# Optimization experiments

Hardware: AMD Instinct MI355X
Metric: run time of the kernel (lower is better)

## Reference

```python
import jax, jax.numpy as jnp
import numpy as np

jax.config.update("jax_enable_x64", True)

N_NODES = 1_000_000
N_EDGES = 16_000_000
N_FEAT = 8
N_LABELS = 16

# odd 64-bit mixing constants (fit in signed int64)
_C1 = jnp.int64(6364136223846793005)
_C2 = jnp.int64(1442695040888963407)
_C3 = jnp.int64(2862933555777941757)
_C4 = jnp.int64(3202034522624059733)
_P_TUPLE = jnp.int64(1000003)  # CPython tuple-hash style prime


def setup_inputs() -> dict:
    key = jax.random.key(0)
    k1, k2 = jax.random.split(key)
    x = jax.random.randint(k1, (N_NODES, N_FEAT), 0, N_LABELS, dtype=jnp.int64)
    edge_index = jax.random.randint(k2, (2, N_EDGES), 0, N_NODES, dtype=jnp.int64)
    return {"x": x, "edge_index": edge_index}


def _mix(h, c1, c2):
    # splitmix-style avalanche; int64 arithmetic wraps, which is fine for hashing
    h = h * c1
    h = h ^ (h >> 31)
    h = h * c2
    return h ^ (h >> 29)


def reference(x, edge_index):
    """One Weisfeiler-Lehman refinement step.

    Faithful to WLConvMultiFeature: each node's new label is determined by
    (own feature tuple, sorted multiset of neighbor feature tuples), relabeled
    to contiguous ids in order of first appearance over nodes 0..N-1.
    Python tuple-hashing is replaced by a vectorized 64-bit hash; the sorted
    neighbor tuple is replaced by an order-invariant (commutative) multiset
    hash, which induces the same node partition up to hash collisions.
    """
    N = x.shape[0]

    # --- hash each feature row -> single int64 label (stand-in for tuple(row))
    lab = jnp.zeros((N,), jnp.int64)
    for j in range(x.shape[1]):  # small fixed loop over feature columns
        lab = lab * _P_TUPLE + x[:, j]
    lab = _mix(lab, _C1, _C2)

    # --- commutative multiset hash of neighbor labels per destination node
    src, dst = edge_index[0], edge_index[1]
    nl = lab[src]  # neighbor (source) labels per edge, shape (E,)
    s1 = jax.ops.segment_sum(_mix(nl, _C1, _C2), dst, num_segments=N)
    s2 = jax.ops.segment_sum(_mix(nl, _C3, _C4), dst, num_segments=N)

    # --- combine own label with neighbor multiset hash
    h = _mix(lab * _C3 + s1, _C1, _C2) ^ _mix(s2 + lab, _C3, _C4)

    # --- relabel hashes to contiguous ids in first-appearance order
    order = jnp.argsort(h, stable=True)          # stable -> first occurrence first
    hs = h[order]
    is_new = jnp.concatenate([jnp.ones((1,), bool), hs[1:] != hs[:-1]])
    gid_sorted = jnp.cumsum(is_new.astype(jnp.int64)) - 1  # group id per sorted pos
    gid = jnp.zeros((N,), jnp.int64).at[order].set(gid_sorted)
    # first original index at which each group appears (padded groups -> int64 max)
    first_idx = jax.ops.segment_min(order, gid_sorted, num_segments=N)
    rank_order = jnp.argsort(first_idx)          # groups sorted by first appearance
    rank = jnp.zeros((N,), jnp.int64).at[rank_order].set(jnp.arange(N, dtype=jnp.int64))
    return rank[gid]
```

## Files before the change

kernel.cpp:

```cpp
#include <hip/hip_runtime.h>
#include <stdint.h>


#define KC1 6364136223846793005ULL
#define KC2 1442695040888963407ULL
#define KC3 2862933555777941757ULL
#define KC4 3202034522624059733ULL
#define KPT 1000003ULL

#define TBL_BITS 21
#define TBL (1u << TBL_BITS)
#define TMASK (TBL - 1u)
#define KEMPTY 0xFFFFFFFFFFFFFFFFULL
#define SIGMASK 0xFFFFFFFFFFF00000ULL

#define BK_SHIFT 12
#define BK_NODES 4096
#define NBK_MAX 256
#define NPARTX 8
#define NPARTS 4
#define NPARTS_LOG 2
#define PCAP 2132u
#define OVFCAP 32768u

#define TILE 16384
#define SUBP 4

typedef int iv4 __attribute__((ext_vector_type(4)));

__device__ __forceinline__ uint64_t mix64(uint64_t h, uint64_t a, uint64_t b) {
    h *= a;
    h ^= (uint64_t)(((int64_t)h) >> 31);
    h *= b;
    h ^= (uint64_t)(((int64_t)h) >> 29);
    return h;
}

__device__ __forceinline__ uint32_t tslot(uint64_t k) {
    return (uint32_t)((k * 0x9E3779B97F4A7C15ULL) >> (64 - TBL_BITS));
}

__device__ __forceinline__ uint32_t psel(uint32_t src, uint32_t M) {
    uint32_t p = (uint32_t)(((uint64_t)src * (uint64_t)M) >> 38);
    return p < (NPARTS - 1) ? p : (NPARTS - 1);
}

__global__ void k_lab(const int* __restrict__ x, uint64_t* __restrict__ lab, int N, int F) {
    int i = blockIdx.x * blockDim.x + threadIdx.x;
    if (i >= N) return;
    const int* row = x + (size_t)i * (size_t)F;
    uint64_t l = 0;
    for (int j = 0; j < F; ++j) l = l * KPT + (uint64_t)(int64_t)row[j];
    lab[i] = mix64(l, KC1, KC2);
}

__global__ __launch_bounds__(1024)
void k_scatter(const int* __restrict__ ei, uint32_t* __restrict__ binned,
               uint32_t* __restrict__ cursor, unsigned long long* __restrict__ ovf,
               unsigned int* __restrict__ ovf_cnt, int E, int NBK, int chunk,
               uint32_t M) {
    __shared__ uint32_t stageRec[TILE];
    __shared__ unsigned short stageCell[TILE];
    __shared__ uint32_t hist[NPARTS * NBK_MAX];
    __shared__ uint32_t cstart[NPARTS * NBK_MAX];
    __shared__ uint32_t lbrun[NPARTS * NBK_MAX];
    const int ncl = NPARTS * NBK;
    const int part = blockIdx.x & (NPARTX - 1);
    const int tid = threadIdx.x;
    const int b0 = blockIdx.x * chunk;
    const int b1 = min(E, b0 + chunk);
    if (b0 >= b1) return;

    if (tid < ncl) hist[tid] = 0;
    __syncthreads();

    for (int tb = b0; tb < b1; tb += TILE) {
        const int tE = min(TILE, b1 - tb);
        uint32_t rc[SUBP * 4];
        uint32_t meta[SUBP * 4];
#pragma unroll
        for (int sidx = 0; sidx < SUBP; ++sidx) {
            const int base = tb + sidx * 4096 + tid * 4;
            int ss[4], dd[4];
            int m = 0;
            if (base + 4 <= min(b1, tb + TILE)) {
                iv4 s4 = __builtin_nontemporal_load((const iv4*)(ei + base));
                iv4 d4 = __builtin_nontemporal_load((const iv4*)(ei + (size_t)E + base));
                ss[0]=s4.x; ss[1]=s4.y; ss[2]=s4.z; ss[3]=s4.w;
                dd[0]=d4.x; dd[1]=d4.y; dd[2]=d4.z; dd[3]=d4.w;
                m = 4;
            } else {
                int lim = min(b1, tb + TILE) - base;
                m = lim > 0 ? (lim < 4 ? lim : 4) : 0;
                for (int j = 0; j < m; ++j) {
                    ss[j] = ei[base + j];
                    dd[j] = ei[(size_t)E + base + j];
                }
            }
#pragma unroll
            for (int j = 0; j < 4; ++j) {
                const int k = sidx * 4 + j;
                if (j < m) {
                    uint32_t bk = (uint32_t)dd[j] >> BK_SHIFT;
                    uint32_t cell = (bk << NPARTS_LOG) | psel((uint32_t)ss[j], M);
                    uint32_t pos = atomicAdd(&hist[cell], 1u);
                    rc[k] = ((uint32_t)(dd[j] & (BK_NODES - 1)) << 20) | (uint32_t)ss[j];
                    meta[k] = (cell << 14) | pos;
                } else {
                    meta[k] = 0xFFFFFFFFu;
                }
            }
        }
        __syncthreads();
        cstart[tid] = (tid < ncl) ? hist[tid] : 0u;
        __syncthreads();
        for (int off = 1; off < 1024; off <<= 1) {
            uint32_t t = (tid >= off) ? cstart[tid - off] : 0u;
            __syncthreads();
            cstart[tid] += t;
            __syncthreads();
        }
        if (tid < ncl) {
            uint32_t c = hist[tid];
            cstart[tid] -= c;
            lbrun[tid] = c ? atomicAdd(&cursor[part * ncl + tid], c) : 0u;
        }
        __syncthreads();
#pragma unroll
        for (int k = 0; k < SUBP * 4; ++k) {
            if (meta[k] != 0xFFFFFFFFu) {
                uint32_t cell = meta[k] >> 14;
                uint32_t p = cstart[cell] + (meta[k] & 0x3FFFu);
                stageRec[p] = rc[k];
                stageCell[p] = (unsigned short)cell;
            }
        }
        __syncthreads();
        for (int i = tid; i < tE; i += 1024) {
            uint32_t rec = stageRec[i];
            uint32_t c = stageCell[i];
            uint32_t idx = lbrun[c] + ((uint32_t)i - cstart[c]);
            if (idx < PCAP) {
                binned[((size_t)part * ncl + c) * PCAP + idx] = rec;
            } else {
                unsigned int o = atomicAdd(ovf_cnt, 1u);
                if (o < OVFCAP) ovf[o] = ((unsigned long long)(c >> NPARTS_LOG) << 32) | rec;
            }
        }
        if (tid < ncl) hist[tid] = 0;
        __syncthreads();
    }
}

__device__ __forceinline__ void acc_rec(unsigned long long* s1,
                                        const uint64_t* __restrict__ lab,
                                        uint32_t rec) {
    uint64_t nl = lab[rec & 0xFFFFFu];
    atomicAdd(&s1[rec >> 20], (unsigned long long)mix64(nl, KC1, KC2));
}

__global__ __launch_bounds__(1024)
void k_accum(const uint32_t* __restrict__ binned, const uint32_t* __restrict__ cursor,
             const unsigned long long* __restrict__ ovf, const unsigned int* __restrict__ ovf_cnt,
             const uint64_t* __restrict__ lab, unsigned long long* __restrict__ table,
             uint32_t* __restrict__ slot32, int N, int NBK) {
    __shared__ unsigned long long s1[BK_NODES];
    const int ncl = NPARTS * NBK;
    int b = blockIdx.x;
    for (int t = threadIdx.x; t < BK_NODES; t += blockDim.x) s1[t] = 0ULL;
    __syncthreads();
    const int xp = threadIdx.x >> 7;
    const int lt = threadIdx.x & 127;
    for (int sp = 0; sp < NPARTS; ++sp) {
        const uint32_t cell = ((uint32_t)b << NPARTS_LOG) | (uint32_t)sp;
        const size_t cidx = (size_t)xp * ncl + cell;
        uint32_t cnt = cursor[cidx];
        if (cnt > PCAP) cnt = PCAP;
        const uint32_t* seg = binned + cidx * PCAP;
        uint32_t i = (uint32_t)lt * 4u;
        for (; i + 3u * 512u + 4u <= cnt; i += 4u * 512u) {
            iv4 r0 = __builtin_nontemporal_load((const iv4*)(seg + i));
            iv4 r1 = __builtin_nontemporal_load((const iv4*)(seg + i + 512u));
            iv4 r2 = __builtin_nontemporal_load((const iv4*)(seg + i + 1024u));
            iv4 r3 = __builtin_nontemporal_load((const iv4*)(seg + i + 1536u));
            uint32_t rr[16];
            rr[0]=(uint32_t)r0.x;  rr[1]=(uint32_t)r0.y;  rr[2]=(uint32_t)r0.z;  rr[3]=(uint32_t)r0.w;
            rr[4]=(uint32_t)r1.x;  rr[5]=(uint32_t)r1.y;  rr[6]=(uint32_t)r1.z;  rr[7]=(uint32_t)r1.w;
            rr[8]=(uint32_t)r2.x;  rr[9]=(uint32_t)r2.y;  rr[10]=(uint32_t)r2.z; rr[11]=(uint32_t)r2.w;
            rr[12]=(uint32_t)r3.x; rr[13]=(uint32_t)r3.y; rr[14]=(uint32_t)r3.z; rr[15]=(uint32_t)r3.w;
            uint64_t lv[16];
#pragma unroll
            for (int k = 0; k < 16; ++k) lv[k] = lab[rr[k] & 0xFFFFFu];
#pragma unroll
            for (int k = 0; k < 16; ++k)
                atomicAdd(&s1[rr[k] >> 20], (unsigned long long)mix64(lv[k], KC1, KC2));
        }
        for (; i < cnt; i += 512u) {
            if (i + 4u <= cnt) {
                iv4 r4 = __builtin_nontemporal_load((const iv4*)(seg + i));
                acc_rec(s1, lab, (uint32_t)r4.x);
                acc_rec(s1, lab, (uint32_t)r4.y);
                acc_rec(s1, lab, (uint32_t)r4.z);
                acc_rec(s1, lab, (uint32_t)r4.w);
            } else {
                for (uint32_t j = i; j < cnt; ++j) acc_rec(s1, lab, seg[j]);
            }
        }
        __syncthreads();
    }
    uint32_t oc = *ovf_cnt;
    if (oc > OVFCAP) oc = OVFCAP;
    for (uint32_t i = threadIdx.x; i < oc; i += blockDim.x) {
        unsigned long long r = ovf[i];
        if ((uint32_t)(r >> 32) == (uint32_t)b) acc_rec(s1, lab, (uint32_t)r);
    }
    __syncthreads();
    int node0 = b << BK_SHIFT;
    for (int t = threadIdx.x; t < BK_NODES; t += blockDim.x) {
        int node = node0 + t;
        if (node < N) {
            uint64_t l = lab[node];
            uint64_t s = (uint64_t)s1[t];
            uint64_t h = mix64(l * KC3 + s, KC1, KC2) ^ mix64(s + l, KC3, KC4);
            uint64_t entry = (h & SIGMASK) | (uint64_t)(uint32_t)node;
            uint32_t slot = tslot(h);
            for (;;) {
                unsigned long long cur = table[slot];
                if (cur == KEMPTY) {
                    unsigned long long prev =
                        atomicCAS(&table[slot], KEMPTY, (unsigned long long)entry);
                    if (prev == KEMPTY) break;
                    cur = prev;
                }
                if ((cur & SIGMASK) == (entry & SIGMASK)) {
                    atomicMin(&table[slot], (unsigned long long)entry);
                    break;
                }
                slot = (slot + 1u) & TMASK;
            }
            slot32[node] = slot;
        }
    }
}

__global__ __launch_bounds__(1024)
void k_lookup_scan(const uint32_t* __restrict__ slot32, const unsigned long long* __restrict__ table,
                   unsigned int* __restrict__ rep, int* __restrict__ incl,
                   int* __restrict__ bsums, int N) {
    __shared__ int wsum[16];
    int tid = threadIdx.x;
    int lane = tid & 63;
    int wid = tid >> 6;
    int i = blockIdx.x * 1024 + tid;
    int v = 0;
    if (i < N) {
        unsigned long long e = table[slot32[i]];
        unsigned int r = (unsigned int)(e & 0xFFFFFu);
        rep[i] = r;
        v = (r == (unsigned int)i) ? 1 : 0;
    }
    int s = v;
#pragma unroll
    for (int off = 1; off < 64; off <<= 1) {
        int t = __shfl_up(s, off, 64);
        if (lane >= off) s += t;
    }
    if (lane == 63) wsum[wid] = s;
    __syncthreads();
    if (wid == 0) {
        int w = (lane < 16) ? wsum[lane] : 0;
#pragma unroll
        for (int off = 1; off < 16; off <<= 1) {
            int t = __shfl_up(w, off, 64);
            if (lane >= off) w += t;
        }
        if (lane < 16) wsum[lane] = w;
    }
    __syncthreads();
    int inclv = s + ((wid > 0) ? wsum[wid - 1] : 0);
    if (i < N) incl[i] = inclv;
    if (tid == 1023) bsums[blockIdx.x] = inclv;
}

__global__ void k_scan2(const int* __restrict__ bsums, int* __restrict__ boffs, int NB) {
    __shared__ int sm[1024];
    int tid = threadIdx.x;
    int v = (tid < NB) ? bsums[tid] : 0;
    sm[tid] = v;
    __syncthreads();
    for (int off = 1; off < 1024; off <<= 1) {
        int t = (tid >= off) ? sm[tid - off] : 0;
        __syncthreads();
        sm[tid] += t;
        __syncthreads();
    }
    if (tid < NB) boffs[tid] = sm[tid] - v;
}

__global__ void k_final(const unsigned int* __restrict__ rep, const int* __restrict__ incl,
                        const int* __restrict__ boffs, int* __restrict__ out, int N) {
    int i = blockIdx.x * blockDim.x + threadIdx.x;
    if (i >= N) return;
    unsigned int r = rep[i];
    out[i] = incl[r] + boffs[r >> 10] - 1;
}

extern "C" void kernel_launch(void* const* d_in, const int* in_sizes, int n_in,
                              void* d_out, int out_size, void* d_ws, size_t ws_size,
                              hipStream_t stream) {
    const int* x  = (const int*)d_in[0];
    const int* ei = (const int*)d_in[1];
    int N = out_size;
    int F = in_sizes[0] / N;
    int E = in_sizes[1] / 2;
    int* out = (int*)d_out;

    int NBK = (N + BK_NODES - 1) >> BK_SHIFT;
    uint32_t PSZ = (uint32_t)((N + NPARTS - 1) / NPARTS);
    uint32_t M = (uint32_t)(((1ULL << 38) + PSZ - 1) / PSZ);

    char* w = (char*)d_ws;
    uint64_t* lab = (uint64_t*)w;                        w += (size_t)N * 8;
    uint32_t* slot32 = (uint32_t*)w;                     w += (size_t)N * 4;
    uint32_t* cursor = (uint32_t*)w;                     w += (size_t)NPARTX * NPARTS * NBK_MAX * 4;
    unsigned int* ovf_cnt = (unsigned int*)w;            w += 16;
    unsigned long long* ovf = (unsigned long long*)w;    w += (size_t)OVFCAP * 8;
    unsigned long long* table = (unsigned long long*)w;  w += (size_t)TBL * 8;
    uint32_t* binned = (uint32_t*)w;
    char* a = (char*)binned;
    unsigned int* rep = (unsigned int*)a;                a += (size_t)N * 4;
    int* incl = (int*)a;                                 a += (size_t)N * 4;
    int* bsums = (int*)a;                                a += 1024 * 4;
    int* boffs = (int*)a;                                a += 1024 * 4;

    int nb = (N + 255) / 256;
    int NB = (N + 1023) / 1024;
    int SCB = 256;
    int chunk = ((E + SCB - 1) / SCB + 3) & ~3;

    (void)hipMemsetAsync(cursor, 0, (size_t)NPARTX * NPARTS * NBK_MAX * 4 + 16, stream);
    (void)hipMemsetAsync(table, 0xFF, (size_t)TBL * 8, stream);
    k_lab<<<nb, 256, 0, stream>>>(x, lab, N, F);
    k_scatter<<<SCB, 1024, 0, stream>>>(ei, binned, cursor, ovf, ovf_cnt, E, NBK, chunk, M);
    k_accum<<<NBK, 1024, 0, stream>>>(binned, cursor, ovf, ovf_cnt, lab, table, slot32, N, NBK);
    k_lookup_scan<<<NB, 1024, 0, stream>>>(slot32, table, rep, incl, bsums, N);
    k_scan2<<<1, 1024, 0, stream>>>(bsums, boffs, NB);
    k_final<<<nb, 256, 0, stream>>>(rep, incl, boffs, out, N);
}
```

Measured before the change: 431.4 us.

## Shrink scatter tile, use wave-shuffle scan, precompute bin addresses, simplify accum loop

The scatter kernel halves its tile and staging depth. It replaces the 10-step shared-memory block scan with a wave-level shuffle scan plus a small cross-wave scan. Final global bin addresses and overflow handling are now computed before staging, so the write-out loop only copies packed 64-bit address/record pairs. The accumulate kernel drops its 16-wide manual unroll for a simpler unroll-2 loop and removes the per-partition barrier, which cuts register pressure and synchronisation but may reduce memory-level parallelism.

```diff
diff --git a/kernel.cpp b/kernel.cpp
--- a/kernel.cpp
+++ b/kernel.cpp
@@ -23,8 +23,8 @@
 #define PCAP 2132u
 #define OVFCAP 32768u
 
-#define TILE 16384
-#define SUBP 4
+#define TILE 8192
+#define SUBP 2
 
 typedef int iv4 __attribute__((ext_vector_type(4)));
 
@@ -59,14 +59,17 @@
                uint32_t* __restrict__ cursor, unsigned long long* __restrict__ ovf,
                unsigned int* __restrict__ ovf_cnt, int E, int NBK, int chunk,
                uint32_t M) {
-    __shared__ uint32_t stageRec[TILE];
-    __shared__ unsigned short stageCell[TILE];
+    __shared__ unsigned long long stagePk[TILE];
     __shared__ uint32_t hist[NPARTS * NBK_MAX];
     __shared__ uint32_t cstart[NPARTS * NBK_MAX];
     __shared__ uint32_t lbrun[NPARTS * NBK_MAX];
+    __shared__ uint32_t wsum[16];
     const int ncl = NPARTS * NBK;
     const int part = blockIdx.x & (NPARTX - 1);
     const int tid = threadIdx.x;
+    const int lane = tid & 63;
+    const int wid = tid >> 6;
+    const size_t partBase = (size_t)part * ncl * PCAP;
     const int b0 = blockIdx.x * chunk;
     const int b1 = min(E, b0 + chunk);
     if (b0 >= b1) return;
@@ -76,6 +79,7 @@
 
     for (int tb = b0; tb < b1; tb += TILE) {
         const int tE = min(TILE, b1 - tb);
+        const int lim = min(b1, tb + TILE);
         uint32_t rc[SUBP * 4];
         uint32_t meta[SUBP * 4];
 #pragma unroll
@@ -83,15 +87,15 @@
             const int base = tb + sidx * 4096 + tid * 4;
             int ss[4], dd[4];
             int m = 0;
-            if (base + 4 <= min(b1, tb + TILE)) {
+            if (base + 4 <= lim) {
                 iv4 s4 = __builtin_nontemporal_load((const iv4*)(ei + base));
                 iv4 d4 = __builtin_nontemporal_load((const iv4*)(ei + (size_t)E + base));
                 ss[0]=s4.x; ss[1]=s4.y; ss[2]=s4.z; ss[3]=s4.w;
                 dd[0]=d4.x; dd[1]=d4.y; dd[2]=d4.z; dd[3]=d4.w;
                 m = 4;
             } else {
-                int lim = min(b1, tb + TILE) - base;
-                m = lim > 0 ? (lim < 4 ? lim : 4) : 0;
+                int r = lim - base;
+                m = r > 0 ? (r < 4 ? r : 4) : 0;
                 for (int j = 0; j < m; ++j) {
                     ss[j] = ei[base + j];
                     dd[j] = ei[(size_t)E + base + j];
@@ -105,47 +109,61 @@
                     uint32_t cell = (bk << NPARTS_LOG) | psel((uint32_t)ss[j], M);
                     uint32_t pos = atomicAdd(&hist[cell], 1u);
                     rc[k] = ((uint32_t)(dd[j] & (BK_NODES - 1)) << 20) | (uint32_t)ss[j];
-                    meta[k] = (cell << 14) | pos;
+                    meta[k] = (cell << 13) | pos;
                 } else {
                     meta[k] = 0xFFFFFFFFu;
                 }
             }
         }
         __syncthreads();
-        cstart[tid] = (tid < ncl) ? hist[tid] : 0u;
-        __syncthreads();
-        for (int off = 1; off < 1024; off <<= 1) {
-            uint32_t t = (tid >= off) ? cstart[tid - off] : 0u;
-            __syncthreads();
-            cstart[tid] += t;
-            __syncthreads();
-        }
+        uint32_t v = (tid < ncl) ? hist[tid] : 0u;
+        uint32_t s = v;
+#pragma unroll
+        for (int off = 1; off < 64; off <<= 1) {
+            uint32_t t = __shfl_up(s, off, 64);
+            if (lane >= off) s += t;
+        }
+        if (lane == 63) wsum[wid] = s;
+        __syncthreads();
+        if (wid == 0) {
+            uint32_t w = (lane < 16) ? wsum[lane] : 0u;
+#pragma unroll
+            for (int off = 1; off < 16; off <<= 1) {
+                uint32_t t = __shfl_up(w, off, 64);
+                if (lane >= off) w += t;
+            }
+            if (lane < 16) wsum[lane] = w;
+        }
+        __syncthreads();
+        uint32_t incl = s + ((wid > 0) ? wsum[wid - 1] : 0u);
         if (tid < ncl) {
-            uint32_t c = hist[tid];
-            cstart[tid] -= c;
-            lbrun[tid] = c ? atomicAdd(&cursor[part * ncl + tid], c) : 0u;
+            cstart[tid] = incl - v;
+            lbrun[tid] = v ? atomicAdd(&cursor[part * ncl + tid], v) : 0u;
         }
         __syncthreads();
 #pragma unroll
         for (int k = 0; k < SUBP * 4; ++k) {
             if (meta[k] != 0xFFFFFFFFu) {
-                uint32_t cell = meta[k] >> 14;
-                uint32_t p = cstart[cell] + (meta[k] & 0x3FFFu);
-                stageRec[p] = rc[k];
-                stageCell[p] = (unsigned short)cell;
+                uint32_t cell = meta[k] >> 13;
+                uint32_t pos  = meta[k] & 0x1FFFu;
+                uint32_t idx = lbrun[cell] + pos;
+                uint32_t p = cstart[cell] + pos;
+                if (idx < PCAP) {
+                    stagePk[p] = ((unsigned long long)(cell * PCAP + idx) << 32) | rc[k];
+                } else {
+                    unsigned int o = atomicAdd(ovf_cnt, 1u);
+                    if (o < OVFCAP)
+                        ovf[o] = ((unsigned long long)(cell >> NPARTS_LOG) << 32) | rc[k];
+                    stagePk[p] = 0xFFFFFFFF00000000ULL | rc[k];
+                }
             }
         }
         __syncthreads();
         for (int i = tid; i < tE; i += 1024) {
-            uint32_t rec = stageRec[i];
-            uint32_t c = stageCell[i];
-            uint32_t idx = lbrun[c] + ((uint32_t)i - cstart[c]);
-            if (idx < PCAP) {
-                binned[((size_t)part * ncl + c) * PCAP + idx] = rec;
-            } else {
-                unsigned int o = atomicAdd(ovf_cnt, 1u);
-                if (o < OVFCAP) ovf[o] = ((unsigned long long)(c >> NPARTS_LOG) << 32) | rec;
-            }
+            unsigned long long pk = stagePk[i];
+            uint32_t addr = (uint32_t)(pk >> 32);
+            if (addr != 0xFFFFFFFFu)
+                binned[partBase + addr] = (uint32_t)pk;
         }
         if (tid < ncl) hist[tid] = 0;
         __syncthreads();
@@ -177,25 +195,8 @@
         uint32_t cnt = cursor[cidx];
         if (cnt > PCAP) cnt = PCAP;
         const uint32_t* seg = binned + cidx * PCAP;
-        uint32_t i = (uint32_t)lt * 4u;
-        for (; i + 3u * 512u + 4u <= cnt; i += 4u * 512u) {
-            iv4 r0 = __builtin_nontemporal_load((const iv4*)(seg + i));
-            iv4 r1 = __builtin_nontemporal_load((const iv4*)(seg + i + 512u));
-            iv4 r2 = __builtin_nontemporal_load((const iv4*)(seg + i + 1024u));
-            iv4 r3 = __builtin_nontemporal_load((const iv4*)(seg + i + 1536u));
-            uint32_t rr[16];
-            rr[0]=(uint32_t)r0.x;  rr[1]=(uint32_t)r0.y;  rr[2]=(uint32_t)r0.z;  rr[3]=(uint32_t)r0.w;
-            rr[4]=(uint32_t)r1.x;  rr[5]=(uint32_t)r1.y;  rr[6]=(uint32_t)r1.z;  rr[7]=(uint32_t)r1.w;
-            rr[8]=(uint32_t)r2.x;  rr[9]=(uint32_t)r2.y;  rr[10]=(uint32_t)r2.z; rr[11]=(uint32_t)r2.w;
-            rr[12]=(uint32_t)r3.x; rr[13]=(uint32_t)r3.y; rr[14]=(uint32_t)r3.z; rr[15]=(uint32_t)r3.w;
-            uint64_t lv[16];
-#pragma unroll
-            for (int k = 0; k < 16; ++k) lv[k] = lab[rr[k] & 0xFFFFFu];
-#pragma unroll
-            for (int k = 0; k < 16; ++k)
-                atomicAdd(&s1[rr[k] >> 20], (unsigned long long)mix64(lv[k], KC1, KC2));
-        }
-        for (; i < cnt; i += 512u) {
+#pragma unroll 2
+        for (uint32_t i = (uint32_t)lt * 4u; i < cnt; i += 512u) {
             if (i + 4u <= cnt) {
                 iv4 r4 = __builtin_nontemporal_load((const iv4*)(seg + i));
                 acc_rec(s1, lab, (uint32_t)r4.x);
@@ -206,7 +207,6 @@
                 for (uint32_t j = i; j < cnt; ++j) acc_rec(s1, lab, seg[j]);
             }
         }
-        __syncthreads();
     }
     uint32_t oc = *ovf_cnt;
     if (oc > OVFCAP) oc = OVFCAP;
```

New measurement: 458.1 us. +6.2%, slower.
